# Kernel tuning notes

Hardware: AMD Instinct MI355X
Metric: run time of the kernel (lower is better)

Reference implementation:

```python
import jax, jax.numpy as jnp
import numpy as np

N_NODES = 20000
N_EDGES = 320000
IN_DIM = 256
HID = 128
HEADS = 4
NEG_SLOPE = 0.2


def _init_params(key):
    ks = jax.random.split(key, 16)
    s1 = 1.0 / np.sqrt(IN_DIM)
    s2 = 1.0 / np.sqrt(HID * HEADS)
    s3 = 1.0 / np.sqrt(HID)
    p = {
        # conv1: GATv2Conv(IN_DIM, HID, heads=HEADS, concat=True)
        'W1l': jax.random.normal(ks[0], (IN_DIM, HEADS * HID), jnp.float32) * s1,
        'b1l': jnp.zeros((HEADS * HID,), jnp.float32),
        'W1r': jax.random.normal(ks[1], (IN_DIM, HEADS * HID), jnp.float32) * s1,
        'b1r': jnp.zeros((HEADS * HID,), jnp.float32),
        'att1': jax.random.normal(ks[2], (HEADS, HID), jnp.float32) * s3,
        'bias1': jnp.zeros((HEADS * HID,), jnp.float32),
        # conv2: GATv2Conv(HID*HEADS, HID, heads=1, concat=False)
        'W2l': jax.random.normal(ks[3], (HID * HEADS, HID), jnp.float32) * s2,
        'b2l': jnp.zeros((HID,), jnp.float32),
        'W2r': jax.random.normal(ks[4], (HID * HEADS, HID), jnp.float32) * s2,
        'b2r': jnp.zeros((HID,), jnp.float32),
        'att2': jax.random.normal(ks[5], (1, HID), jnp.float32) * s3,
        'bias2': jnp.zeros((HID,), jnp.float32),
        # heads
        'Wa': jax.random.normal(ks[6], (HID, 1), jnp.float32) * s3,
        'ba': jnp.zeros((1,), jnp.float32),
        'Wrc': jax.random.normal(ks[7], (HID, 1), jnp.float32) * s3,
        'brc': jnp.zeros((1,), jnp.float32),
    }
    return p


def setup_inputs() -> dict:
    key = jax.random.key(0)
    kx, ke, kp = jax.random.split(key, 3)
    inp = {
        'x': jax.random.normal(kx, (N_NODES, IN_DIM), jnp.float32),
        'edge_index': jax.random.randint(ke, (2, N_EDGES), 0, N_NODES, jnp.int64),
    }
    inp.update(_init_params(kp))
    return inp


def _gatv2(x, Wl, bl, Wr, br, att, bias, src, dst, heads, out_ch, concat):
    # GATv2: e_ij = att . leaky_relu(lin_l(x_j) + lin_r(x_i)), softmax over dst,
    # out_i = sum_j alpha_ij * lin_l(x_j)
    n = x.shape[0]
    xl = (x @ Wl + bl).reshape(n, heads, out_ch)  # source transform
    xr = (x @ Wr + br).reshape(n, heads, out_ch)  # target transform
    e = jax.nn.leaky_relu(xl[src] + xr[dst], NEG_SLOPE)  # [E,H,C]
    score = jnp.einsum('ehc,hc->eh', e, att)              # [E,H]
    smax = jax.ops.segment_max(score, dst, num_segments=n)  # [N,H]
    ex = jnp.exp(score - smax[dst])
    denom = jax.ops.segment_sum(ex, dst, num_segments=n)
    alpha = ex / (denom[dst] + 1e-16)                     # [E,H]
    msg = alpha[..., None] * xl[src]                      # [E,H,C]
    out = jax.ops.segment_sum(msg, dst, num_segments=n)   # [N,H,C]
    if concat:
        out = out.reshape(n, heads * out_ch)
    else:
        out = out.mean(axis=1)
    return out + bias


def reference(x, edge_index, W1l, b1l, W1r, b1r, att1, bias1,
              W2l, b2l, W2r, b2r, att2, bias2, Wa, ba, Wrc, brc):
    src, dst = edge_index[0], edge_index[1]
    h = _gatv2(x, W1l, b1l, W1r, b1r, att1, bias1, src, dst, HEADS, HID, True)
    h = jax.nn.elu(h)
    # dropout p=0.2 is identity in eval mode
    h = _gatv2(h, W2l, b2l, W2r, b2r, att2, bias2, src, dst, 1, HID, False)
    anomaly = jax.nn.sigmoid(h @ Wa + ba)
    root_cause = jax.nn.sigmoid(h @ Wrc + brc)
    return anomaly, root_cause
```

## Files before the change

### kernel.cpp

```cpp
#include <hip/hip_runtime.h>
#include <hip/hip_bf16.h>

#define N_NODES 20000
#define N_EDGES 320000
#define IN_DIM 256
#define HID 128
#define HEADS 4
#define MPAD 20096

typedef unsigned short u16;
typedef __attribute__((ext_vector_type(8))) short bf16x8;
typedef __attribute__((ext_vector_type(4))) float f32x4;
typedef __attribute__((address_space(1))) void g_void;
typedef __attribute__((address_space(3))) void l_void;

__device__ __forceinline__ float asf(unsigned int u) {
    union { unsigned int i; float f; } c; c.i = u; return c.f;
}
__device__ __forceinline__ float bflo(unsigned int u) { return asf(u << 16); }
__device__ __forceinline__ float bfhi(unsigned int u) { return asf(u & 0xffff0000u); }
__device__ __forceinline__ u16 f2bf(float f) {
    union { float f; unsigned int i; } c; c.f = f;
    return (u16)((c.i + 0x7FFF + ((c.i >> 16) & 1)) >> 16);
}
__device__ __forceinline__ int xcd_swz(int orig, int nwg) {
    int q = nwg >> 3, r = nwg & 7;
    int xcd = orig & 7, lin = orig >> 3;
    return (xcd < r ? xcd * (q + 1) : r * (q + 1) + (xcd - r) * q) + lin;
}

__global__ void hist_kernel(const int* __restrict__ dst, int* __restrict__ deg, int E) {
    int i = blockIdx.x * blockDim.x + threadIdx.x;
    if (i < E) atomicAdd(&deg[dst[i]], 1);
}

__global__ __launch_bounds__(1024) void scan_kernel(
    const int* __restrict__ deg, int* __restrict__ row_start,
    int* __restrict__ cursor, int n) {
    __shared__ int partial[1024];
    int t = threadIdx.x;
    int chunk = (n + 1023) / 1024;
    int begin = t * chunk;
    int end = min(begin + chunk, n);
    int s = 0;
    for (int i = begin; i < end; ++i) s += deg[i];
    partial[t] = s;
    __syncthreads();
    for (int off = 1; off < 1024; off <<= 1) {
        int v = (t >= off) ? partial[t - off] : 0;
        __syncthreads();
        partial[t] += v;
        __syncthreads();
    }
    int run = (t == 0) ? 0 : partial[t - 1];
    for (int i = begin; i < end; ++i) {
        row_start[i] = run;
        cursor[i] = run;
        run += deg[i];
    }
    if (t == 1023) row_start[n] = run;
}

__global__ void scatter_kernel(const int* __restrict__ dst, int* __restrict__ cursor,
                               int* __restrict__ seid, int* __restrict__ sdst, int E) {
    int i = blockIdx.x * blockDim.x + threadIdx.x;
    if (i < E) {
        int d = dst[i];
        int pos = atomicAdd(&cursor[d], 1);
        seid[pos] = i;
        sdst[pos] = d;
    }
}

__global__ void rank_kernel(const int* __restrict__ row_start, const int* __restrict__ seid,
                            const int* __restrict__ sdst, const int* __restrict__ src,
                            int* __restrict__ ssrc, int E) {
    int i = blockIdx.x * blockDim.x + threadIdx.x;
    if (i >= E) return;
    int d = sdst[i];
    int beg = row_start[d], end = row_start[d + 1];
    int my = seid[i];
    int rank = 0;
    for (int j = beg; j < end; ++j) rank += (seid[j] < my) ? 1 : 0;
    ssrc[beg + rank] = src[my];
}

__global__ void cast_x_kernel(const float* __restrict__ x, u16* __restrict__ xb) {
    int i = blockIdx.x * blockDim.x + threadIdx.x;
    const int nq = MPAD * IN_DIM / 4;
    if (i >= nq) return;
    int elem = i * 4;
    uint2 u;
    if (elem < N_NODES * IN_DIM) {
        float4 v = ((const float4*)x)[i];
        u.x = (unsigned)f2bf(v.x) | ((unsigned)f2bf(v.y) << 16);
        u.y = (unsigned)f2bf(v.z) | ((unsigned)f2bf(v.w) << 16);
    } else {
        u.x = 0u; u.y = 0u;
    }
    *(uint2*)(xb + elem) = u;
}

__global__ __launch_bounds__(256) void transpose_all_kernel(
    const float* __restrict__ W1l, const float* __restrict__ W1r,
    const float* __restrict__ W2l, const float* __restrict__ W2r,
    u16* __restrict__ BT1, u16* __restrict__ BT2) {
    const float* W; u16* out; int K, N;
    switch (blockIdx.z) {
        case 0:  W = W1l; out = BT1;             K = 256; N = 512; break;
        case 1:  W = W1r; out = BT1 + 512 * 256; K = 256; N = 512; break;
        case 2:  W = W2l; out = BT2;             K = 512; N = 128; break;
        default: W = W2r; out = BT2 + 128 * 512; K = 512; N = 128; break;
    }
    int bx = blockIdx.x * 32;
    int by = blockIdx.y * 32;
    if (bx >= N || by >= K) return;
    __shared__ float t[32][33];
    int tx = threadIdx.x, ty = threadIdx.y;
    #pragma unroll
    for (int j = 0; j < 32; j += 8)
        t[ty + j][tx] = W[(size_t)(by + ty + j) * N + bx + tx];
    __syncthreads();
    #pragma unroll
    for (int j = 0; j < 32; j += 8)
        out[(size_t)(bx + ty + j) * K + by + tx] = f2bf(t[tx][ty + j]);
}

__global__ void prep_bias_kernel(const float* b1l, const float* b1r,
                                 const float* b2l, const float* b2r,
                                 float* bc1, float* bc2) {
    int t = threadIdx.x;
    if (t < 512) bc1[t] = b1l[t];
    else bc1[t] = b1r[t - 512];
    if (t < 128) bc2[t] = b2l[t];
    else if (t < 256) bc2[t] = b2r[t - 128];
}

__global__ __launch_bounds__(256) void gemm_bf16_kernel(
    const u16* __restrict__ A, const u16* __restrict__ BT,
    const float* __restrict__ bias, u16* __restrict__ C,
    int K, int N, int nbx) {
    __shared__ u16 smem[8192];
    u16* As = smem;
    u16* Bs = smem + 4096;
    const int tid = threadIdx.x;
    const int lane = tid & 63;
    const int wid = tid >> 6;
    const int wr = wid >> 1, wc = wid & 1;
    const int wg = xcd_swz(blockIdx.x, gridDim.x);
    const int brow = (wg / nbx) * 128, bcol = (wg % nbx) * 128;

    const int srow = tid >> 2;
    const int skk = (((tid & 3) ^ ((tid >> 3) & 3))) * 8;
    const u16* ga0 = A + (size_t)(brow + srow) * K + skk;
    const u16* ga1 = A + (size_t)(brow + 64 + srow) * K + skk;
    const u16* gb0 = BT + (size_t)(bcol + srow) * K + skk;
    const u16* gb1 = BT + (size_t)(bcol + 64 + srow) * K + skk;
    u16* lA0 = As + tid * 8;
    u16* lA1 = As + 2048 + tid * 8;
    u16* lB0 = Bs + tid * 8;
    u16* lB1 = Bs + 2048 + tid * 8;

    const int fr = lane & 15;
    const int fg = lane >> 4;
    const int fslot = (fg ^ ((fr >> 1) & 3)) * 8;
    const u16* ra = As + (wr * 64 + fr) * 32 + fslot;
    const u16* rb = Bs + (wc * 64 + fr) * 32 + fslot;

    f32x4 acc[4][4];
    #pragma unroll
    for (int m = 0; m < 4; ++m)
        #pragma unroll
        for (int n = 0; n < 4; ++n)
            acc[m][n] = (f32x4){0.f, 0.f, 0.f, 0.f};

    for (int k0 = 0; k0 < K; k0 += 32) {
        __builtin_amdgcn_global_load_lds((const g_void*)(ga0 + k0), (l_void*)lA0, 16, 0, 0);
        __builtin_amdgcn_global_load_lds((const g_void*)(ga1 + k0), (l_void*)lA1, 16, 0, 0);
        __builtin_amdgcn_global_load_lds((const g_void*)(gb0 + k0), (l_void*)lB0, 16, 0, 0);
        __builtin_amdgcn_global_load_lds((const g_void*)(gb1 + k0), (l_void*)lB1, 16, 0, 0);
        __syncthreads();
        bf16x8 av[4], bv[4];
        #pragma unroll
        for (int m = 0; m < 4; ++m) av[m] = *(const bf16x8*)(ra + m * 512);
        #pragma unroll
        for (int n = 0; n < 4; ++n) bv[n] = *(const bf16x8*)(rb + n * 512);
        #pragma unroll
        for (int m = 0; m < 4; ++m)
            #pragma unroll
            for (int n = 0; n < 4; ++n)
                acc[m][n] = __builtin_amdgcn_mfma_f32_16x16x32_bf16(av[m], bv[n], acc[m][n], 0, 0, 0);
        __syncthreads();
    }

    float bv4[4];
    #pragma unroll
    for (int n = 0; n < 4; ++n) bv4[n] = bias[bcol + wc * 64 + n * 16 + fr];
    #pragma unroll
    for (int ph = 0; ph < 2; ++ph) {
        __syncthreads();
        if (wr == ph) {
            #pragma unroll
            for (int m = 0; m < 4; ++m)
                #pragma unroll
                for (int n = 0; n < 4; ++n) {
                    const int cc = wc * 64 + n * 16 + fr;
                    #pragma unroll
                    for (int j = 0; j < 4; ++j) {
                        const int rr = m * 16 + fg * 4 + j;
                        smem[rr * 128 + (cc ^ (((rr >> 2) & 3) << 4))] =
                            f2bf(acc[m][n][j] + bv4[n]);
                    }
                }
        }
        __syncthreads();
        #pragma unroll
        for (int it = 0; it < 4; ++it) {
            const int rr = it * 16 + (tid >> 4);
            const int cc0 = (tid & 15) * 8;
            *(bf16x8*)(C + (size_t)(brow + ph * 64 + rr) * N + bcol + cc0) =
                *(const bf16x8*)(smem + rr * 128 + (cc0 ^ (((rr >> 2) & 3) << 4)));
        }
    }
}

#define UNPACK8(c, f) \
    f[0] = bflo(c.x); f[1] = bfhi(c.x); f[2] = bflo(c.y); f[3] = bfhi(c.y); \
    f[4] = bflo(c.z); f[5] = bfhi(c.z); f[6] = bflo(c.w); f[7] = bfhi(c.w);

__global__ __launch_bounds__(256) void fused1_kernel(
    const u16* __restrict__ xlr, const int* __restrict__ row_start,
    const int* __restrict__ ssrc, const float* __restrict__ att1,
    const float* __restrict__ bias1, u16* __restrict__ h1, int n) {
    int node = blockIdx.x * 4 + (threadIdx.x >> 6);
    int lane = threadIdx.x & 63;
    if (node >= n) return;

    uint4 xr4 = *(const uint4*)(xlr + (size_t)node * 1024 + 512 + lane * 8);
    float xrf[8];
    UNPACK8(xr4, xrf);
    float4 w0 = ((const float4*)att1)[lane * 2];
    float4 w1 = ((const float4*)att1)[lane * 2 + 1];
    float wa[8] = {w0.x, w0.y, w0.z, w0.w, w1.x, w1.y, w1.z, w1.w};

    int beg = row_start[node], end = row_start[node + 1];
    float l = 0.f;
    float acc[8] = {0.f, 0.f, 0.f, 0.f, 0.f, 0.f, 0.f, 0.f};

    uint4 v0 = {0, 0, 0, 0}, v1 = {0, 0, 0, 0};
    if (beg < end)     v0 = *(const uint4*)(xlr + (size_t)ssrc[beg] * 1024 + lane * 8);
    if (beg + 1 < end) v1 = *(const uint4*)(xlr + (size_t)ssrc[beg + 1] * 1024 + lane * 8);

    for (int p = beg; p < end; p += 2) {
        uint4 c0 = v0, c1 = v1;
        if (p + 2 < end) v0 = *(const uint4*)(xlr + (size_t)ssrc[p + 2] * 1024 + lane * 8);
        if (p + 3 < end) v1 = *(const uint4*)(xlr + (size_t)ssrc[p + 3] * 1024 + lane * 8);

        float xf[8];
        UNPACK8(c0, xf);
        float sc = 0.f;
        #pragma unroll
        for (int j = 0; j < 8; ++j) {
            float v = xf[j] + xrf[j];
            sc = fmaf(fmaxf(v, 0.2f * v), wa[j], sc);
        }
        sc += __shfl_xor(sc, 1);
        sc += __shfl_xor(sc, 2);
        sc += __shfl_xor(sc, 4);
        sc += __shfl_xor(sc, 8);
        float pv = __expf(sc);
        l += pv;
        #pragma unroll
        for (int j = 0; j < 8; ++j) acc[j] = fmaf(pv, xf[j], acc[j]);

        if (p + 1 < end) {
            float yf[8];
            UNPACK8(c1, yf);
            float sc1 = 0.f;
            #pragma unroll
            for (int j = 0; j < 8; ++j) {
                float v = yf[j] + xrf[j];
                sc1 = fmaf(fmaxf(v, 0.2f * v), wa[j], sc1);
            }
            sc1 += __shfl_xor(sc1, 1);
            sc1 += __shfl_xor(sc1, 2);
            sc1 += __shfl_xor(sc1, 4);
            sc1 += __shfl_xor(sc1, 8);
            float pv1 = __expf(sc1);
            l += pv1;
            #pragma unroll
            for (int j = 0; j < 8; ++j) acc[j] = fmaf(pv1, yf[j], acc[j]);
        }
    }

    float inv = 1.f / (l + 1e-16f);
    float4 b0 = ((const float4*)bias1)[lane * 2];
    float4 b1 = ((const float4*)bias1)[lane * 2 + 1];
    float bb[8] = {b0.x, b0.y, b0.z, b0.w, b1.x, b1.y, b1.z, b1.w};
    bf16x8 outv;
    #pragma unroll
    for (int j = 0; j < 8; ++j) {
        float v = fmaf(acc[j], inv, bb[j]);
        v = v > 0.f ? v : __expf(v) - 1.f;
        outv[j] = (short)f2bf(v);
    }
    *(bf16x8*)(h1 + (size_t)node * 512 + lane * 8) = outv;
}

__global__ __launch_bounds__(256) void fused2_kernel(
    const u16* __restrict__ xlr2, const int* __restrict__ row_start,
    const int* __restrict__ ssrc, const float* __restrict__ att2,
    const float* __restrict__ bias2, const float* __restrict__ Wa,
    const float* __restrict__ ba, const float* __restrict__ Wrc,
    const float* __restrict__ brc, float* __restrict__ out, int n) {
    int node = blockIdx.x * 4 + (threadIdx.x >> 6);
    int lane = threadIdx.x & 63;
    if (node >= n) return;

    unsigned int xr = *(const unsigned int*)(xlr2 + (size_t)node * 256 + 128 + lane * 2);
    float xr0 = bflo(xr), xr1 = bfhi(xr);
    float2 w = ((const float2*)att2)[lane];

    int beg = row_start[node], end = row_start[node + 1];
    float l = 0.f, acc0 = 0.f, acc1 = 0.f;

    unsigned int v0 = 0, v1 = 0;
    if (beg < end)     v0 = *(const unsigned int*)(xlr2 + (size_t)ssrc[beg] * 256 + lane * 2);
    if (beg + 1 < end) v1 = *(const unsigned int*)(xlr2 + (size_t)ssrc[beg + 1] * 256 + lane * 2);

    for (int p = beg; p < end; p += 2) {
        unsigned int c0 = v0, c1 = v1;
        if (p + 2 < end) v0 = *(const unsigned int*)(xlr2 + (size_t)ssrc[p + 2] * 256 + lane * 2);
        if (p + 3 < end) v1 = *(const unsigned int*)(xlr2 + (size_t)ssrc[p + 3] * 256 + lane * 2);

        float x0 = bflo(c0), x1 = bfhi(c0);
        float t0 = x0 + xr0, t1 = x1 + xr1;
        float sc = fmaxf(t0, 0.2f * t0) * w.x + fmaxf(t1, 0.2f * t1) * w.y;
        #pragma unroll
        for (int off = 1; off < 64; off <<= 1) sc += __shfl_xor(sc, off);
        float pv = __expf(sc);
        l += pv;
        acc0 = fmaf(pv, x0, acc0);
        acc1 = fmaf(pv, x1, acc1);

        if (p + 1 < end) {
            float y0 = bflo(c1), y1 = bfhi(c1);
            float u0 = y0 + xr0, u1 = y1 + xr1;
            float sc1 = fmaxf(u0, 0.2f * u0) * w.x + fmaxf(u1, 0.2f * u1) * w.y;
            #pragma unroll
            for (int off = 1; off < 64; off <<= 1) sc1 += __shfl_xor(sc1, off);
            float pv1 = __expf(sc1);
            l += pv1;
            acc0 = fmaf(pv1, y0, acc0);
            acc1 = fmaf(pv1, y1, acc1);
        }
    }

    float inv = 1.f / (l + 1e-16f);
    int c0i = lane * 2, c1i = lane * 2 + 1;
    float h0 = fmaf(acc0, inv, bias2[c0i]);
    float h1v = fmaf(acc1, inv, bias2[c1i]);
    float a = h0 * Wa[c0i] + h1v * Wa[c1i];
    float r = h0 * Wrc[c0i] + h1v * Wrc[c1i];
    #pragma unroll
    for (int off = 1; off < 64; off <<= 1) {
        a += __shfl_xor(a, off);
        r += __shfl_xor(r, off);
    }
    if (lane == 0) {
        out[node]     = 1.f / (1.f + __expf(-(a + ba[0])));
        out[n + node] = 1.f / (1.f + __expf(-(r + brc[0])));
    }
}

extern "C" void kernel_launch(void* const* d_in, const int* in_sizes, int n_in,
                              void* d_out, int out_size, void* d_ws, size_t ws_size,
                              hipStream_t stream) {
    const float* x    = (const float*)d_in[0];
    const int* ei     = (const int*)d_in[1];
    const float* W1l  = (const float*)d_in[2];
    const float* b1l  = (const float*)d_in[3];
    const float* W1r  = (const float*)d_in[4];
    const float* b1r  = (const float*)d_in[5];
    const float* att1 = (const float*)d_in[6];
    const float* bias1= (const float*)d_in[7];
    const float* W2l  = (const float*)d_in[8];
    const float* b2l  = (const float*)d_in[9];
    const float* W2r  = (const float*)d_in[10];
    const float* b2r  = (const float*)d_in[11];
    const float* att2 = (const float*)d_in[12];
    const float* bias2= (const float*)d_in[13];
    const float* Wa   = (const float*)d_in[14];
    const float* ba   = (const float*)d_in[15];
    const float* Wrc  = (const float*)d_in[16];
    const float* brc  = (const float*)d_in[17];
    float* out = (float*)d_out;

    const int N = N_NODES, E = N_EDGES;
    const int* src = ei;
    const int* dst = ei + E;

    char* ws = (char*)d_ws;
    u16*   xlr1 = (u16*)ws;
    u16*   h1b  = (u16*)(ws + 41156608);
    u16*   xb   = (u16*)(ws + 61734912);
    u16*   xlr2 = (u16*)(ws + 61734912);
    u16*   BT1  = (u16*)(ws + 72024064);
    u16*   BT2  = (u16*)(ws + 72548352);
    float* bc1  = (float*)(ws + 72810496);
    float* bc2  = (float*)(ws + 72814592);
    int* deg       = (int*)(ws + 72815616);
    int* row_start = (int*)(ws + 72896000);
    int* cursor    = (int*)(ws + 72976128);
    int* ssrc      = (int*)(ws + 73056128);
    int* seid      = (int*)(ws + 74336128);
    int* sdst      = (int*)(ws + 75616128);

    hipMemsetAsync(deg, 0, N * sizeof(int), stream);
    hist_kernel<<<(E + 255) / 256, 256, 0, stream>>>(dst, deg, E);
    scan_kernel<<<1, 1024, 0, stream>>>(deg, row_start, cursor, N);
    scatter_kernel<<<(E + 255) / 256, 256, 0, stream>>>(dst, cursor, seid, sdst, E);
    rank_kernel<<<(E + 255) / 256, 256, 0, stream>>>(row_start, seid, sdst, src, ssrc, E);

    cast_x_kernel<<<(MPAD * IN_DIM / 4 + 255) / 256, 256, 0, stream>>>(x, xb);
    transpose_all_kernel<<<dim3(16, 16, 4), dim3(32, 8), 0, stream>>>(
        W1l, W1r, W2l, W2r, BT1, BT2);
    prep_bias_kernel<<<1, 1024, 0, stream>>>(b1l, b1r, b2l, b2r, bc1, bc2);

    gemm_bf16_kernel<<<157 * 8, 256, 0, stream>>>(xb, BT1, bc1, xlr1, 256, 1024, 8);
    fused1_kernel<<<(N + 3) / 4, 256, 0, stream>>>(xlr1, row_start, ssrc, att1, bias1, h1b, N);

    gemm_bf16_kernel<<<157 * 2, 256, 0, stream>>>(h1b, BT2, bc2, xlr2, 512, 256, 2);
    fused2_kernel<<<(N + 3) / 4, 256, 0, stream>>>(xlr2, row_start, ssrc, att2, bias2,
                                                   Wa, ba, Wrc, brc, out, N);
}
```

Measured before the change: 227.7 us.

## Split each node's edge list across two wavefronts and merge partials in LDS

Both fused aggregation kernels now assign two wavefronts per destination node. Each wave handles alternating edges and keeps its own accumulators, and the partial sums and softmax denominators are combined through shared memory after a block barrier. The goal is more memory-level parallelism on the gather loads and shorter per-wave loops, so latency hides better. In exchange the launch uses twice as many waves per node, adds an LDS round trip and a __syncthreads, and drops the node-bounds check because N is even.

```diff
diff --git a/kernel.cpp b/kernel.cpp
--- a/kernel.cpp
+++ b/kernel.cpp
@@ -231,10 +231,14 @@
 __global__ __launch_bounds__(256) void fused1_kernel(
     const u16* __restrict__ xlr, const int* __restrict__ row_start,
     const int* __restrict__ ssrc, const float* __restrict__ att1,
-    const float* __restrict__ bias1, u16* __restrict__ h1, int n) {
-    int node = blockIdx.x * 4 + (threadIdx.x >> 6);
-    int lane = threadIdx.x & 63;
-    if (node >= n) return;
+    const float* __restrict__ bias1, u16* __restrict__ h1) {
+    __shared__ float part[2][64][9];
+    const int tid = threadIdx.x;
+    const int wid = tid >> 6;
+    const int nsub = wid >> 1;
+    const int wsub = wid & 1;
+    const int node = blockIdx.x * 2 + nsub;
+    const int lane = tid & 63;
 
     uint4 xr4 = *(const uint4*)(xlr + (size_t)node * 1024 + 512 + lane * 8);
     float xrf[8];
@@ -243,18 +247,19 @@
     float4 w1 = ((const float4*)att1)[lane * 2 + 1];
     float wa[8] = {w0.x, w0.y, w0.z, w0.w, w1.x, w1.y, w1.z, w1.w};
 
-    int beg = row_start[node], end = row_start[node + 1];
+    const int beg = row_start[node], end = row_start[node + 1];
     float l = 0.f;
     float acc[8] = {0.f, 0.f, 0.f, 0.f, 0.f, 0.f, 0.f, 0.f};
 
+    const int p0 = beg + wsub;
     uint4 v0 = {0, 0, 0, 0}, v1 = {0, 0, 0, 0};
-    if (beg < end)     v0 = *(const uint4*)(xlr + (size_t)ssrc[beg] * 1024 + lane * 8);
-    if (beg + 1 < end) v1 = *(const uint4*)(xlr + (size_t)ssrc[beg + 1] * 1024 + lane * 8);
-
-    for (int p = beg; p < end; p += 2) {
+    if (p0 < end)     v0 = *(const uint4*)(xlr + (size_t)ssrc[p0] * 1024 + lane * 8);
+    if (p0 + 2 < end) v1 = *(const uint4*)(xlr + (size_t)ssrc[p0 + 2] * 1024 + lane * 8);
+
+    for (int p = p0; p < end; p += 4) {
         uint4 c0 = v0, c1 = v1;
-        if (p + 2 < end) v0 = *(const uint4*)(xlr + (size_t)ssrc[p + 2] * 1024 + lane * 8);
-        if (p + 3 < end) v1 = *(const uint4*)(xlr + (size_t)ssrc[p + 3] * 1024 + lane * 8);
+        if (p + 4 < end) v0 = *(const uint4*)(xlr + (size_t)ssrc[p + 4] * 1024 + lane * 8);
+        if (p + 6 < end) v1 = *(const uint4*)(xlr + (size_t)ssrc[p + 6] * 1024 + lane * 8);
 
         float xf[8];
         UNPACK8(c0, xf);
@@ -273,7 +278,7 @@
         #pragma unroll
         for (int j = 0; j < 8; ++j) acc[j] = fmaf(pv, xf[j], acc[j]);
 
-        if (p + 1 < end) {
+        if (p + 2 < end) {
             float yf[8];
             UNPACK8(c1, yf);
             float sc1 = 0.f;
@@ -293,18 +298,30 @@
         }
     }
 
-    float inv = 1.f / (l + 1e-16f);
-    float4 b0 = ((const float4*)bias1)[lane * 2];
-    float4 b1 = ((const float4*)bias1)[lane * 2 + 1];
-    float bb[8] = {b0.x, b0.y, b0.z, b0.w, b1.x, b1.y, b1.z, b1.w};
-    bf16x8 outv;
-    #pragma unroll
-    for (int j = 0; j < 8; ++j) {
-        float v = fmaf(acc[j], inv, bb[j]);
-        v = v > 0.f ? v : __expf(v) - 1.f;
-        outv[j] = (short)f2bf(v);
-    }
-    *(bf16x8*)(h1 + (size_t)node * 512 + lane * 8) = outv;
+    if (wsub == 1) {
+        #pragma unroll
+        for (int j = 0; j < 8; ++j) part[nsub][lane][j] = acc[j];
+        part[nsub][lane][8] = l;
+    }
+    __syncthreads();
+    if (wsub == 0) {
+        #pragma unroll
+        for (int j = 0; j < 8; ++j) acc[j] += part[nsub][lane][j];
+        l += part[nsub][lane][8];
+
+        float inv = 1.f / (l + 1e-16f);
+        float4 b0 = ((const float4*)bias1)[lane * 2];
+        float4 b1 = ((const float4*)bias1)[lane * 2 + 1];
+        float bb[8] = {b0.x, b0.y, b0.z, b0.w, b1.x, b1.y, b1.z, b1.w};
+        bf16x8 outv;
+        #pragma unroll
+        for (int j = 0; j < 8; ++j) {
+            float v = fmaf(acc[j], inv, bb[j]);
+            v = v > 0.f ? v : __expf(v) - 1.f;
+            outv[j] = (short)f2bf(v);
+        }
+        *(bf16x8*)(h1 + (size_t)node * 512 + lane * 8) = outv;
+    }
 }
 
 __global__ __launch_bounds__(256) void fused2_kernel(
@@ -313,25 +330,30 @@
     const float* __restrict__ bias2, const float* __restrict__ Wa,
     const float* __restrict__ ba, const float* __restrict__ Wrc,
     const float* __restrict__ brc, float* __restrict__ out, int n) {
-    int node = blockIdx.x * 4 + (threadIdx.x >> 6);
-    int lane = threadIdx.x & 63;
-    if (node >= n) return;
+    __shared__ float part[2][64][3];
+    const int tid = threadIdx.x;
+    const int wid = tid >> 6;
+    const int nsub = wid >> 1;
+    const int wsub = wid & 1;
+    const int node = blockIdx.x * 2 + nsub;
+    const int lane = tid & 63;
 
     unsigned int xr = *(const unsigned int*)(xlr2 + (size_t)node * 256 + 128 + lane * 2);
     float xr0 = bflo(xr), xr1 = bfhi(xr);
     float2 w = ((const float2*)att2)[lane];
 
-    int beg = row_start[node], end = row_start[node + 1];
+    const int beg = row_start[node], end = row_start[node + 1];
     float l = 0.f, acc0 = 0.f, acc1 = 0.f;
 
+    const int p0 = beg + wsub;
     unsigned int v0 = 0, v1 = 0;
-    if (beg < end)     v0 = *(const unsigned int*)(xlr2 + (size_t)ssrc[beg] * 256 + lane * 2);
-    if (beg + 1 < end) v1 = *(const unsigned int*)(xlr2 + (size_t)ssrc[beg + 1] * 256 + lane * 2);
-
-    for (int p = beg; p < end; p += 2) {
+    if (p0 < end)     v0 = *(const unsigned int*)(xlr2 + (size_t)ssrc[p0] * 256 + lane * 2);
+    if (p0 + 2 < end) v1 = *(const unsigned int*)(xlr2 + (size_t)ssrc[p0 + 2] * 256 + lane * 2);
+
+    for (int p = p0; p < end; p += 4) {
         unsigned int c0 = v0, c1 = v1;
-        if (p + 2 < end) v0 = *(const unsigned int*)(xlr2 + (size_t)ssrc[p + 2] * 256 + lane * 2);
-        if (p + 3 < end) v1 = *(const unsigned int*)(xlr2 + (size_t)ssrc[p + 3] * 256 + lane * 2);
+        if (p + 4 < end) v0 = *(const unsigned int*)(xlr2 + (size_t)ssrc[p + 4] * 256 + lane * 2);
+        if (p + 6 < end) v1 = *(const unsigned int*)(xlr2 + (size_t)ssrc[p + 6] * 256 + lane * 2);
 
         float x0 = bflo(c0), x1 = bfhi(c0);
         float t0 = x0 + xr0, t1 = x1 + xr1;
@@ -343,7 +365,7 @@
         acc0 = fmaf(pv, x0, acc0);
         acc1 = fmaf(pv, x1, acc1);
 
-        if (p + 1 < end) {
+        if (p + 2 < end) {
             float y0 = bflo(c1), y1 = bfhi(c1);
             float u0 = y0 + xr0, u1 = y1 + xr1;
             float sc1 = fmaxf(u0, 0.2f * u0) * w.x + fmaxf(u1, 0.2f * u1) * w.y;
@@ -356,20 +378,32 @@
         }
     }
 
-    float inv = 1.f / (l + 1e-16f);
-    int c0i = lane * 2, c1i = lane * 2 + 1;
-    float h0 = fmaf(acc0, inv, bias2[c0i]);
-    float h1v = fmaf(acc1, inv, bias2[c1i]);
-    float a = h0 * Wa[c0i] + h1v * Wa[c1i];
-    float r = h0 * Wrc[c0i] + h1v * Wrc[c1i];
-    #pragma unroll
-    for (int off = 1; off < 64; off <<= 1) {
-        a += __shfl_xor(a, off);
-        r += __shfl_xor(r, off);
-    }
-    if (lane == 0) {
-        out[node]     = 1.f / (1.f + __expf(-(a + ba[0])));
-        out[n + node] = 1.f / (1.f + __expf(-(r + brc[0])));
+    if (wsub == 1) {
+        part[nsub][lane][0] = acc0;
+        part[nsub][lane][1] = acc1;
+        part[nsub][lane][2] = l;
+    }
+    __syncthreads();
+    if (wsub == 0) {
+        acc0 += part[nsub][lane][0];
+        acc1 += part[nsub][lane][1];
+        l += part[nsub][lane][2];
+
+        float inv = 1.f / (l + 1e-16f);
+        int c0i = lane * 2, c1i = lane * 2 + 1;
+        float h0 = fmaf(acc0, inv, bias2[c0i]);
+        float h1v = fmaf(acc1, inv, bias2[c1i]);
+        float a = h0 * Wa[c0i] + h1v * Wa[c1i];
+        float r = h0 * Wrc[c0i] + h1v * Wrc[c1i];
+        #pragma unroll
+        for (int off = 1; off < 64; off <<= 1) {
+            a += __shfl_xor(a, off);
+            r += __shfl_xor(r, off);
+        }
+        if (lane == 0) {
+            out[node]     = 1.f / (1.f + __expf(-(a + ba[0])));
+            out[n + node] = 1.f / (1.f + __expf(-(r + brc[0])));
+        }
     }
 }
 
@@ -428,9 +462,9 @@
     prep_bias_kernel<<<1, 1024, 0, stream>>>(b1l, b1r, b2l, b2r, bc1, bc2);
 
     gemm_bf16_kernel<<<157 * 8, 256, 0, stream>>>(xb, BT1, bc1, xlr1, 256, 1024, 8);
-    fused1_kernel<<<(N + 3) / 4, 256, 0, stream>>>(xlr1, row_start, ssrc, att1, bias1, h1b, N);
+    fused1_kernel<<<N / 2, 256, 0, stream>>>(xlr1, row_start, ssrc, att1, bias1, h1b);
 
     gemm_bf16_kernel<<<157 * 2, 256, 0, stream>>>(h1b, BT2, bc2, xlr2, 512, 256, 2);
-    fused2_kernel<<<(N + 3) / 4, 256, 0, stream>>>(xlr2, row_start, ssrc, att2, bias2,
-                                                   Wa, ba, Wrc, brc, out, N);
-}
+    fused2_kernel<<<N / 2, 256, 0, stream>>>(xlr2, row_start, ssrc, att2, bias2,
+                                             Wa, ba, Wrc, brc, out, N);
+}
```

Measured after the change: 228.2 us. No clear change (+0.2%).
